# Optimization experiments

Measured on AMD Instinct MI355X. Metric: run time of the kernel, lower is better.

The kernel has to match this reference:

```python
import jax, jax.numpy as jnp
import numpy as np

B, S, DIM, NH, NKV, HD, HID, L, VOCAB = 1, 2048, 1024, 16, 8, 64, 2816, 2, 32000
EPS = 1e-5
SCALE = float(HD) ** 0.5
NEG = -255.0  # mask fill value used by executorch example inputs


def setup_inputs() -> dict:
    key = jax.random.key(0)
    ks = jax.random.split(key, 16)
    sd = 0.02
    def rnd(k, shape):
        return jax.random.normal(k, shape, dtype=jnp.float32) * sd
    # rope tables: precompute_freqs_cis(head_dim, max_seq_len)[: -1] -> [S, HD//2]
    inv = 1.0 / (10000.0 ** (np.arange(0, HD, 2, dtype=np.float32) / HD))
    ang = np.outer(np.arange(S, dtype=np.float32), inv)
    # causal mask [S, S]
    tril = np.tril(np.ones((S, S), dtype=bool))
    mask = np.where(tril, 0.0, NEG).astype(np.float32)
    return {
        "tokens": jax.random.randint(ks[0], (B, S), 0, VOCAB, dtype=jnp.int32),
        "atten_mask": jnp.asarray(mask),
        "freqs_cos": jnp.asarray(np.cos(ang)),
        "freqs_sin": jnp.asarray(np.sin(ang)),
        "tok_emb": rnd(ks[1], (VOCAB, DIM)),
        "wq": rnd(ks[2], (L, DIM, NH * HD)),
        "wk": rnd(ks[3], (L, DIM, NKV * HD)),
        "wv": rnd(ks[4], (L, DIM, NKV * HD)),
        "wo": rnd(ks[5], (L, NH * HD, DIM)),
        "attn_norm_w": jnp.ones((L, DIM), jnp.float32),
        "ffn_norm_w": jnp.ones((L, DIM), jnp.float32),
        "w1": rnd(ks[6], (L, DIM, HID)),
        "w2": rnd(ks[7], (L, HID, DIM)),
        "w3": rnd(ks[8], (L, DIM, HID)),
        "final_norm_w": jnp.ones((DIM,), jnp.float32),
        "out_w": rnd(ks[9], (DIM, VOCAB)),
    }


def _rmsnorm(x, w):
    return x * jax.lax.rsqrt(jnp.mean(x * x, axis=-1, keepdims=True) + EPS) * w


def _rope(x, c, s):
    # faithful to apply_rotary_emb_single: de-interleave, rotate, concat halves
    xr, xi = x[..., ::2], x[..., 1::2]          # [B,S,H,HD/2]
    c = c[None, :, None, :]
    s = s[None, :, None, :]
    return jnp.concatenate([xr * c - xi * s, xr * s + xi * c], axis=-1)


def reference(tokens, atten_mask, freqs_cos, freqs_sin, tok_emb, wq, wk, wv, wo,
              attn_norm_w, ffn_norm_w, w1, w2, w3, final_norm_w, out_w):
    rep = NH // NKV
    h = tok_emb[tokens]                           # [B,S,DIM]
    k_news, v_news = [], []
    for l in range(L):
        x = _rmsnorm(h, attn_norm_w[l])
        q = (x @ wq[l]).reshape(B, S, NH, HD)
        k = (x @ wk[l]).reshape(B, S, NKV, HD)
        v = (x @ wv[l]).reshape(B, S, NKV, HD)
        q = _rope(q, freqs_cos, freqs_sin)
        k = _rope(k, freqs_cos, freqs_sin)
        # GQA: each kv head serves NH//NKV query heads
        kr = jnp.repeat(k, rep, axis=2)           # [B,S,NH,HD]
        vr = jnp.repeat(v, rep, axis=2)
        attn = jnp.einsum('bshd,bthd->bhst', q, kr) / SCALE + atten_mask[None, None]
        p = jax.nn.softmax(attn, axis=-1)
        y = jnp.einsum('bhst,bthd->bshd', p, vr).reshape(B, S, NH * HD)
        h = h + y @ wo[l]
        x = _rmsnorm(h, ffn_norm_w[l])
        h = h + (jax.nn.silu(x @ w1[l]) * (x @ w3[l])) @ w2[l]
        # output_new_cache_only: last-position rotated K and raw V per kv head
        k_news.append(k[:, -1])                   # [B,NKV,HD]
        v_news.append(v[:, -1])
    logits = _rmsnorm(h, final_norm_w) @ out_w    # [B,S,VOCAB]
    return logits, jnp.stack(k_news), jnp.stack(v_news)
```

## Files before the change

kernel.cpp:

```cpp
#include <hip/hip_runtime.h>
#include <hip/hip_bf16.h>

typedef __bf16 bf16x8 __attribute__((ext_vector_type(8)));
typedef float f32x4 __attribute__((ext_vector_type(4)));
typedef unsigned short ushort4v __attribute__((ext_vector_type(4)));
typedef unsigned short ushort8v __attribute__((ext_vector_type(8)));

#define S_LEN 2048
#define DIM 1024
#define NH 16
#define NKV 8
#define HD 64
#define HID 2816
#define LOGITS ((size_t)S_LEN * 32000)

__device__ __forceinline__ unsigned short f2bf(float f) {
    union { float f; unsigned u; } v; v.f = f;
    unsigned r = v.u + 0x7fffu + ((v.u >> 16) & 1u);
    return (unsigned short)(r >> 16);
}
__device__ __forceinline__ float bf2f(unsigned short u) {
    union { unsigned u; float f; } v; v.u = (unsigned)u << 16; return v.f;
}

__device__ __forceinline__ void gload16(const unsigned short* g, unsigned short* l) {
    __builtin_amdgcn_global_load_lds(
        (const __attribute__((address_space(1))) unsigned int*)g,
        (__attribute__((address_space(3))) unsigned int*)l,
        16, 0, 0);
}

union Frag { f32x4 f; bf16x8 h; };

__device__ __forceinline__ f32x4 lds_read_b128(unsigned addr) {
    f32x4 d;
    asm volatile("ds_read_b128 %0, %1" : "=v"(d) : "v"(addr));
    return d;
}

#define BAR()  asm volatile("s_barrier" ::: "memory")
#define WAITV(n) asm volatile("s_waitcnt vmcnt(" #n ")" ::: "memory")
#define LGKM0() do { asm volatile("s_waitcnt lgkmcnt(0)" ::: "memory"); __builtin_amdgcn_sched_barrier(0); } while (0)

__global__ __launch_bounds__(256) void embed_kernel(const int* __restrict__ tokens,
                                                    const float* __restrict__ emb,
                                                    float* __restrict__ h) {
    int s = blockIdx.x;
    int t = tokens[s];
    float4 v = *(const float4*)&emb[(size_t)t * DIM + threadIdx.x * 4];
    *(float4*)&h[(size_t)s * DIM + threadIdx.x * 4] = v;
}

__global__ __launch_bounds__(256) void rmsnorm_kernel(const float* __restrict__ x,
                                                      const float* __restrict__ w,
                                                      unsigned short* __restrict__ out) {
    __shared__ float sred[4];
    int s = blockIdx.x;
    int tid = threadIdx.x;
    float4 v = *(const float4*)&x[(size_t)s * DIM + tid * 4];
    float ss = v.x * v.x + v.y * v.y + v.z * v.z + v.w * v.w;
#pragma unroll
    for (int off = 32; off; off >>= 1) ss += __shfl_down(ss, off);
    if ((tid & 63) == 0) sred[tid >> 6] = ss;
    __syncthreads();
    float tot = sred[0] + sred[1] + sred[2] + sred[3];
    float scale = rsqrtf(tot * (1.0f / DIM) + 1e-5f);
    float4 wv = *(const float4*)&w[tid * 4];
    ushort4v o;
    o[0] = f2bf(v.x * scale * wv.x); o[1] = f2bf(v.y * scale * wv.y);
    o[2] = f2bf(v.z * scale * wv.z); o[3] = f2bf(v.w * scale * wv.w);
    *(ushort4v*)&out[(size_t)s * DIM + tid * 4] = o;
}

__device__ __forceinline__ void tpose_body(const float* __restrict__ in,
                                           unsigned short* __restrict__ out,
                                           int K, int N, int n0, int k0,
                                           int rowMul, int rowOff) {
    __shared__ unsigned short t[64][68];
    int tid = threadIdx.x;
    int tn = tid & 15, tk = tid >> 4;
#pragma unroll
    for (int p = 0; p < 4; ++p) {
        int k = tk + p * 16;
        float4 v = *(const float4*)&in[(size_t)(k0 + k) * N + n0 + tn * 4];
        t[tn * 4 + 0][k] = f2bf(v.x);
        t[tn * 4 + 1][k] = f2bf(v.y);
        t[tn * 4 + 2][k] = f2bf(v.z);
        t[tn * 4 + 3][k] = f2bf(v.w);
    }
    __syncthreads();
    int wk = tid & 15, wn = tid >> 4;
#pragma unroll
    for (int p = 0; p < 4; ++p) {
        int n = wn + p * 16;
        ushort4v v;
        v[0] = t[n][wk * 4]; v[1] = t[n][wk * 4 + 1];
        v[2] = t[n][wk * 4 + 2]; v[3] = t[n][wk * 4 + 3];
        *(ushort4v*)&out[(size_t)(rowMul * (n0 + n) + rowOff) * K + k0 + wk * 4] = v;
    }
}

__global__ __launch_bounds__(256) void transpose_w(const float* __restrict__ in,
                                                   unsigned short* __restrict__ out,
                                                   int K, int N) {
    tpose_body(in, out, K, N, blockIdx.x * 64, blockIdx.y * 64, 1, 0);
}

__global__ __launch_bounds__(256) void transpose_qkv(const float* __restrict__ wq,
                                                     const float* __restrict__ wk,
                                                     const float* __restrict__ wv,
                                                     unsigned short* __restrict__ out) {
    int z = blockIdx.z;
    if (z > 0 && blockIdx.x >= 8) return;
    const float* in = z == 0 ? wq : (z == 1 ? wk : wv);
    int N = z == 0 ? 1024 : 512;
    int rowOff = z == 0 ? 0 : (z == 1 ? 1024 : 1536);
    tpose_body(in, out, DIM, N, blockIdx.x * 64, blockIdx.y * 64, 1, rowOff);
}

__global__ __launch_bounds__(256) void transpose_w13(const float* __restrict__ w1,
                                                     const float* __restrict__ w3,
                                                     unsigned short* __restrict__ out) {
    int z = blockIdx.z;
    tpose_body(z ? w3 : w1, out, DIM, HID, blockIdx.x * 64, blockIdx.y * 64, 2, z);
}

__global__ __launch_bounds__(256) void gemm_qkv(const unsigned short* __restrict__ A,
                                                const unsigned short* __restrict__ Bt,
                                                const float* __restrict__ fc,
                                                const float* __restrict__ fs,
                                                unsigned short* __restrict__ qb,
                                                unsigned short* __restrict__ kb,
                                                unsigned short* __restrict__ vT,
                                                float* __restrict__ out, int layer) {
    __shared__ unsigned short As[128 * 64];
    __shared__ unsigned short Bs[128 * 64];
    const int K = DIM, lda = DIM;
    int tid = threadIdx.x;
    int lane = tid & 63;
    int wid = tid >> 6;
    int wrow = wid >> 1, wcol = wid & 1;
    int lr = lane & 15, lg = lane >> 4;
    const int m0 = blockIdx.x * 128, n0 = blockIdx.y * 128;

    const int col8 = (((lane & 7) ^ ((lane >> 3) & 7)) * 8);
    const unsigned short* aG = A + (size_t)(m0 + wid * 32 + (lane >> 3)) * lda + col8;
    const unsigned short* bG = Bt + (size_t)(n0 + wid * 32 + (lane >> 3)) * K + col8;
    unsigned short* aL = As + wid * 2048;
    unsigned short* bL = Bs + wid * 2048;

    f32x4 acc[4][4] = {};

    for (int k0 = 0; k0 < K; k0 += 64) {
#pragma unroll
        for (int i = 0; i < 4; ++i)
            gload16(aG + (size_t)(i * 8) * lda + k0, aL + i * 512);
#pragma unroll
        for (int i = 0; i < 4; ++i)
            gload16(bG + (size_t)(i * 8) * K + k0, bL + i * 512);
        __syncthreads();
#pragma unroll
        for (int kk = 0; kk < 2; ++kk) {
            const int slot = ((kk * 4 + lg) ^ (lr & 7)) * 8;
            bf16x8 aF[4], bF[4];
#pragma unroll
            for (int mi = 0; mi < 4; ++mi)
                aF[mi] = *(const bf16x8*)&As[(wrow * 64 + mi * 16 + lr) * 64 + slot];
#pragma unroll
            for (int ni = 0; ni < 4; ++ni)
                bF[ni] = *(const bf16x8*)&Bs[(wcol * 64 + ni * 16 + lr) * 64 + slot];
#pragma unroll
            for (int mi = 0; mi < 4; ++mi)
#pragma unroll
                for (int ni = 0; ni < 4; ++ni)
                    acc[mi][ni] = __builtin_amdgcn_mfma_f32_16x16x32_bf16(aF[mi], bF[ni], acc[mi][ni], 0, 0, 0);
        }
        __syncthreads();
    }
#pragma unroll
    for (int mi = 0; mi < 4; ++mi)
#pragma unroll
        for (int ni = 0; ni < 4; ++ni) {
            int col = n0 + wcol * 64 + ni * 16 + lr;
            int s0r = m0 + wrow * 64 + mi * 16 + lg * 4;
            if (col < 1536) {
                int p = (col & 63) >> 1;
                int odd = col & 1;
#pragma unroll
                for (int r = 0; r < 4; ++r) {
                    float v = acc[mi][ni][r];
                    float o = __shfl_xor(v, 1);
                    int s = s0r + r;
                    float c = fc[s * 32 + p], sn = fs[s * 32 + p];
                    float res = odd ? (o * sn + v * c) : (v * c - o * sn);
                    int dpos = (odd ? 32 : 0) + p;
                    if (col < 1024) {
                        qb[(size_t)s * 1024 + (col >> 6) * 64 + dpos] = f2bf(res);
                    } else {
                        int kcol = ((col >> 6) - 16) * 64 + dpos;
                        kb[(size_t)s * 512 + kcol] = f2bf(res);
                        if (s == S_LEN - 1)
                            out[LOGITS + (size_t)layer * 512 + kcol] = res;
                    }
                }
            } else {
                int d = col - 1536;
                ushort4v vv;
#pragma unroll
                for (int r = 0; r < 4; ++r) vv[r] = f2bf(acc[mi][ni][r]);
                *(ushort4v*)&vT[(size_t)d * 2048 + s0r] = vv;
                if (s0r + 3 == S_LEN - 1)
                    out[LOGITS + 2 * 512 + (size_t)layer * 512 + d] = acc[mi][ni][3];
            }
        }
}

__global__ __launch_bounds__(256) void gemm_tn64(const unsigned short* __restrict__ A, int lda,
                                                 const unsigned short* __restrict__ Bt,
                                                 float* __restrict__ Cf,
                                                 const float* __restrict__ addsrc,
                                                 int N, int K) {
    __shared__ unsigned short As[64 * 64];
    __shared__ unsigned short Bs[128 * 64];
    int tid = threadIdx.x;
    int lane = tid & 63;
    int wid = tid >> 6;
    int lr = lane & 15, lg = lane >> 4;
    const int m0 = blockIdx.x * 64, n0 = blockIdx.y * 128;

    const int srow = tid >> 3;
    const int col8 = (((tid & 7) ^ ((tid >> 3) & 7)) * 8);
    const unsigned short* aG = A + (size_t)(m0 + srow) * lda + col8;
    const unsigned short* bG = Bt + (size_t)(n0 + srow) * K + col8;
    unsigned short* aL = As + wid * 512;
    unsigned short* bL = Bs + wid * 512;

    f32x4 acc[4][2] = {};

    for (int k0 = 0; k0 < K; k0 += 64) {
        gload16(aG + k0, aL);
        gload16(aG + (size_t)32 * lda + k0, aL + 2048);
#pragma unroll
        for (int i = 0; i < 4; ++i)
            gload16(bG + (size_t)(i * 32) * K + k0, bL + i * 2048);
        __syncthreads();
#pragma unroll
        for (int kk = 0; kk < 2; ++kk) {
            const int slot = ((kk * 4 + lg) ^ (lr & 7)) * 8;
            bf16x8 aF[4], bF[2];
#pragma unroll
            for (int mi = 0; mi < 4; ++mi)
                aF[mi] = *(const bf16x8*)&As[(mi * 16 + lr) * 64 + slot];
#pragma unroll
            for (int ni = 0; ni < 2; ++ni)
                bF[ni] = *(const bf16x8*)&Bs[(wid * 32 + ni * 16 + lr) * 64 + slot];
#pragma unroll
            for (int mi = 0; mi < 4; ++mi)
#pragma unroll
                for (int ni = 0; ni < 2; ++ni)
                    acc[mi][ni] = __builtin_amdgcn_mfma_f32_16x16x32_bf16(aF[mi], bF[ni], acc[mi][ni], 0, 0, 0);
        }
        __syncthreads();
    }
#pragma unroll
    for (int mi = 0; mi < 4; ++mi)
#pragma unroll
        for (int ni = 0; ni < 2; ++ni) {
            int row = m0 + mi * 16 + lg * 4;
            int col = n0 + wid * 32 + ni * 16 + lr;
#pragma unroll
            for (int r = 0; r < 4; ++r) {
                size_t idx = (size_t)(row + r) * N + col;
                float v = acc[mi][ni][r];
                if (addsrc) v += addsrc[idx];
                Cf[idx] = v;
            }
        }
}

template<int FUSE>
__global__ __launch_bounds__(512) void gemm8(const unsigned short* __restrict__ A,
                                             const unsigned short* __restrict__ Bt,
                                             float* __restrict__ Cf,
                                             unsigned short* __restrict__ Cb,
                                             int N, int K) {
    __shared__ unsigned short ldsbuf[65536];
    const int NT = K >> 6;
    int tid = threadIdx.x;
    int lane = tid & 63;
    int wid = tid >> 6;
    int wm = wid >> 2, wn = wid & 3;
    int lr = lane & 15, lg = lane >> 4;
    int wl = blockIdx.x * gridDim.y + blockIdx.y;
    const int m0 = (wl & 7) * 256, n0 = (wl >> 3) * 256;

    unsigned lds0 = (unsigned)(size_t)(__attribute__((address_space(3))) unsigned short*)ldsbuf;
    const unsigned xoff = (unsigned)((lg ^ ((lr >> 1) & 3)) * 16);
    const int gsw = (lane & 3) ^ ((lane >> 3) & 3);
    const int srow = wid * 16 + (lane >> 2);

#define STAGE(buf, ab, s, t) do {                                                   \
        const unsigned short* _src = (ab) ? Bt : A;                                 \
        int _r0 = (ab) ? n0 : m0;                                                   \
        unsigned short* _l = ldsbuf + (((buf) * 2 + (ab)) * 2 + (s)) * 8192 + wid * 512; \
        const unsigned short* _g = _src + (size_t)(_r0 + srow) * K + (size_t)(t) * 64 + (s) * 32 + gsw * 8; \
        gload16(_g, _l);                                                            \
        gload16(_g + (size_t)128 * K, _l + 4096);                                   \
    } while (0)

    f32x4 acc[8][4] = {};

    STAGE(0, 0, 0, 0); STAGE(0, 1, 0, 0);
    STAGE(0, 0, 1, 0); STAGE(0, 1, 1, 0);
    STAGE(1, 0, 0, 1); STAGE(1, 1, 0, 1);
    WAITV(8);
    BAR();

    for (int t = 0; t < NT; ++t) {
        int buf = t & 1;
        unsigned aBase = lds0 + (unsigned)(buf * 65536) + (unsigned)((wm * 128 + lr) * 64) + xoff;
        unsigned bBase = lds0 + (unsigned)(buf * 65536 + 32768) + (unsigned)((wn * 64 + lr) * 64) + xoff;
        Frag aF[4], bF[4];
#pragma unroll
        for (int s = 0; s < 2; ++s) {
#pragma unroll
            for (int ni = 0; ni < 4; ++ni)
                bF[ni].f = lds_read_b128(bBase + (unsigned)(s * 16384 + ni * 1024));
#pragma unroll
            for (int mi = 0; mi < 4; ++mi)
                aF[mi].f = lds_read_b128(aBase + (unsigned)(s * 16384 + mi * 1024));
            if (s == 0) { if (t + 1 < NT) STAGE(buf ^ 1, 0, 1, t + 1); }
            else        { if (t + 2 < NT) STAGE(buf,     0, 0, t + 2); }
            BAR();
            LGKM0();
            __builtin_amdgcn_s_setprio(1);
#pragma unroll
            for (int mi = 0; mi < 4; ++mi)
#pragma unroll
                for (int ni = 0; ni < 4; ++ni)
                    acc[mi][ni] = __builtin_amdgcn_mfma_f32_16x16x32_bf16(aF[mi].h, bF[ni].h, acc[mi][ni], 0, 0, 0);
            __builtin_amdgcn_s_setprio(0);
            BAR();
#pragma unroll
            for (int mi = 0; mi < 4; ++mi)
                aF[mi].f = lds_read_b128(aBase + (unsigned)(4096 + s * 16384 + mi * 1024));
            if (s == 0) { if (t + 1 < NT) STAGE(buf ^ 1, 1, 1, t + 1); }
            else        { if (t + 2 < NT) STAGE(buf,     1, 0, t + 2); }
            BAR();
            LGKM0();
            __builtin_amdgcn_s_setprio(1);
#pragma unroll
            for (int mi = 0; mi < 4; ++mi)
#pragma unroll
                for (int ni = 0; ni < 4; ++ni)
                    acc[4 + mi][ni] = __builtin_amdgcn_mfma_f32_16x16x32_bf16(aF[mi].h, bF[ni].h, acc[4 + mi][ni], 0, 0, 0);
            __builtin_amdgcn_s_setprio(0);
            if (s == 0) {
                if (t + 1 < NT) { WAITV(8); } else { WAITV(0); }
            } else {
                if (t + 2 < NT)      { WAITV(8); }
                else if (t + 1 < NT) { WAITV(4); }
            }
            BAR();
        }
    }
#undef STAGE

#pragma unroll
    for (int mi = 0; mi < 8; ++mi)
#pragma unroll
        for (int ni = 0; ni < 4; ++ni) {
            int row = m0 + wm * 128 + mi * 16 + lg * 4;
            int col = n0 + wn * 64 + ni * 16 + lr;
#pragma unroll
            for (int r = 0; r < 4; ++r) {
                float v = acc[mi][ni][r];
                if (FUSE) {
                    float o = __shfl_xor(v, 1);
                    if (!(lr & 1)) {
                        float res = v / (1.f + __expf(-v)) * o;
                        Cb[(size_t)(row + r) * (HID) + (col >> 1)] = f2bf(res);
                    }
                } else {
                    Cf[(size_t)(row + r) * N + col] = v;
                }
            }
        }
}

__global__ __launch_bounds__(512) void gemm8k32(const unsigned short* __restrict__ A,
                                                const unsigned short* __restrict__ Bt,
                                                float* __restrict__ Cf,
                                                int N, int K) {
    __shared__ unsigned short ldsbuf[32768];
    const int NT = K >> 5;
    int tid = threadIdx.x;
    int lane = tid & 63;
    int wid = tid >> 6;
    int wm = wid >> 2, wn = wid & 3;
    int lr = lane & 15, lg = lane >> 4;
    int wl = blockIdx.x * gridDim.y + blockIdx.y;
    const int m0 = (wl & 7) * 256, n0 = (wl >> 3) * 256;

    unsigned lds0 = (unsigned)(size_t)(__attribute__((address_space(3))) unsigned short*)ldsbuf;
    const unsigned xoff = (unsigned)((lg ^ ((lr >> 1) & 3)) * 16);
    const int gsw = (lane & 3) ^ ((lane >> 3) & 3);
    const int srow = wid * 16 + (lane >> 2);

#define STGA(t) do { \
        unsigned short* _l = ldsbuf + (((t) & 1) * 2 + 0) * 8192 + wid * 512; \
        const unsigned short* _g = A + (size_t)(m0 + srow) * K + (size_t)(t) * 32 + gsw * 8; \
        gload16(_g, _l); \
        gload16(_g + (size_t)128 * K, _l + 4096); \
    } while (0)
#define STGB(t) do { \
        unsigned short* _l = ldsbuf + (((t) & 1) * 2 + 1) * 8192 + wid * 512; \
        const unsigned short* _g = Bt + (size_t)(n0 + srow) * K + (size_t)(t) * 32 + gsw * 8; \
        gload16(_g, _l); \
        gload16(_g + (size_t)128 * K, _l + 4096); \
    } while (0)

    f32x4 acc[8][4] = {};

    STGA(0); STGB(0); STGB(1);
    WAITV(2);
    BAR();

    for (int t = 0; t < NT; ++t) {
        int buf = t & 1;
        unsigned aBase = lds0 + (unsigned)(buf * 32768) + (unsigned)((wm * 128 + lr) * 64) + xoff;
        unsigned bBase = lds0 + (unsigned)(buf * 32768 + 16384) + (unsigned)((wn * 64 + lr) * 64) + xoff;
        Frag aF[4], bF[4];
#pragma unroll
        for (int ni = 0; ni < 4; ++ni)
            bF[ni].f = lds_read_b128(bBase + (unsigned)(ni * 1024));
#pragma unroll
        for (int mi = 0; mi < 4; ++mi)
            aF[mi].f = lds_read_b128(aBase + (unsigned)(mi * 1024));
        if (t + 1 < NT) STGA(t + 1);
        BAR();
        LGKM0();
        __builtin_amdgcn_s_setprio(1);
#pragma unroll
        for (int mi = 0; mi < 4; ++mi)
#pragma unroll
            for (int ni = 0; ni < 4; ++ni)
                acc[mi][ni] = __builtin_amdgcn_mfma_f32_16x16x32_bf16(aF[mi].h, bF[ni].h, acc[mi][ni], 0, 0, 0);
        __builtin_amdgcn_s_setprio(0);
        BAR();
#pragma unroll
        for (int mi = 0; mi < 4; ++mi)
            aF[mi].f = lds_read_b128(aBase + (unsigned)(4096 + mi * 1024));
        if (t + 2 < NT) STGB(t + 2);
        BAR();
        LGKM0();
        __builtin_amdgcn_s_setprio(1);
#pragma unroll
        for (int mi = 0; mi < 4; ++mi)
#pragma unroll
            for (int ni = 0; ni < 4; ++ni)
                acc[4 + mi][ni] = __builtin_amdgcn_mfma_f32_16x16x32_bf16(aF[mi].h, bF[ni].h, acc[4 + mi][ni], 0, 0, 0);
        __builtin_amdgcn_s_setprio(0);
        if (t + 2 < NT)      { WAITV(2); }
        else if (t + 1 < NT) { WAITV(0); }
        BAR();
    }
#undef STGA
#undef STGB

#pragma unroll
    for (int mi = 0; mi < 8; ++mi)
#pragma unroll
        for (int ni = 0; ni < 4; ++ni) {
            int row = m0 + wm * 128 + mi * 16 + lg * 4;
            int col = n0 + wn * 64 + ni * 16 + lr;
#pragma unroll
            for (int r = 0; r < 4; ++r)
                Cf[(size_t)(row + r) * N + col] = acc[mi][ni][r];
        }
}

__global__ __launch_bounds__(256) void attn_kernel(const unsigned short* __restrict__ qb,
                                                   const unsigned short* __restrict__ kb,
                                                   const unsigned short* __restrict__ vT,
                                                   unsigned short* __restrict__ yb) {
    __shared__ unsigned short Klds[2][4096];
    __shared__ unsigned short Vlds[2][4096];
    __shared__ unsigned short P[4][16 * 72];
    int kvh = blockIdx.x;
    int strip = 63 - blockIdx.y;
    int tid = threadIdx.x;
    int lane = tid & 63;
    int w = tid >> 6;
    int hq = w & 1, qsub = w >> 1;
    int h = kvh * 2 + hq;
    int lr = lane & 15, lg = lane >> 4;
    int qbase = strip * 32 + qsub * 16;
    int qrow = qbase + lr;

    const int sr = tid >> 3;
    const int scol8 = (((tid & 7) ^ (sr & 7)) * 8);
    const int NT = (strip >> 1) + 1;

#define STAGEKV(buf, kt) do { \
        gload16(&kb[(size_t)((kt) * 64 + sr) * 512 + kvh * 64 + scol8], &Klds[buf][w * 512]); \
        gload16(&kb[(size_t)((kt) * 64 + sr + 32) * 512 + kvh * 64 + scol8], &Klds[buf][2048 + w * 512]); \
        gload16(&vT[(size_t)(kvh * 64 + sr) * 2048 + (kt) * 64 + scol8], &Vlds[buf][w * 512]); \
        gload16(&vT[(size_t)(kvh * 64 + sr + 32) * 2048 + (kt) * 64 + scol8], &Vlds[buf][2048 + w * 512]); \
    } while (0)

    bf16x8 bq[2];
#pragma unroll
    for (int c = 0; c < 2; ++c)
        bq[c] = *(const bf16x8*)&qb[(size_t)qrow * (NH * HD) + h * HD + c * 32 + lg * 8];

    f32x4 O[4] = {};
    float mstate = -1e30f, lstate = 0.f;

    STAGEKV(0, 0);
    WAITV(0);
    BAR();

    for (int kt = 0; kt < NT; ++kt) {
        int buf = kt & 1;
        if (kt + 1 < NT) STAGEKV(buf ^ 1, kt + 1);
        f32x4 s[4];
#pragma unroll
        for (int kc = 0; kc < 4; ++kc) {
            int krl = kc * 16 + lr;
            const unsigned short* kp = &Klds[buf][krl * 64];
            bf16x8 ak0 = *(const bf16x8*)&kp[((lg ^ (lr & 7)) * 8)];
            bf16x8 ak1 = *(const bf16x8*)&kp[(((4 + lg) ^ (lr & 7)) * 8)];
            f32x4 z = {};
            z = __builtin_amdgcn_mfma_f32_16x16x32_bf16(ak0, bq[0], z, 0, 0, 0);
            z = __builtin_amdgcn_mfma_f32_16x16x32_bf16(ak1, bq[1], z, 0, 0, 0);
            s[kc] = z;
        }
        float tm = -1e30f;
#pragma unroll
        for (int kc = 0; kc < 4; ++kc)
#pragma unroll
            for (int r = 0; r < 4; ++r) {
                int key = kt * 64 + kc * 16 + lg * 4 + r;
                float val = s[kc][r] * 0.125f;
                if (key > qrow) val = -1e30f;
                s[kc][r] = val;
                tm = fmaxf(tm, val);
            }
        tm = fmaxf(tm, __shfl_xor(tm, 16));
        tm = fmaxf(tm, __shfl_xor(tm, 32));
        float mn = fmaxf(mstate, tm);
        float sc = __expf(mstate - mn);
        float rs = 0.f;
        ushort4v pk[4];
#pragma unroll
        for (int kc = 0; kc < 4; ++kc)
#pragma unroll
            for (int r = 0; r < 4; ++r) {
                float pf = __expf(s[kc][r] - mn);
                rs += pf;
                pk[kc][r] = f2bf(pf);
            }
        rs += __shfl_xor(rs, 16);
        rs += __shfl_xor(rs, 32);
        lstate = lstate * sc + rs;
        mstate = mn;
        float osc[4];
#pragma unroll
        for (int r = 0; r < 4; ++r)
            osc[r] = __shfl(sc, lg * 4 + r);
#pragma unroll
        for (int n = 0; n < 4; ++n)
#pragma unroll
            for (int r = 0; r < 4; ++r)
                O[n][r] *= osc[r];
#pragma unroll
        for (int kc = 0; kc < 4; ++kc)
            *(ushort4v*)&P[w][lr * 72 + kc * 16 + lg * 4] = pk[kc];
        bf16x8 pa[2];
#pragma unroll
        for (int g = 0; g < 2; ++g)
            pa[g] = *(const bf16x8*)&P[w][lr * 72 + g * 32 + lg * 8];
#pragma unroll
        for (int n = 0; n < 4; ++n) {
            const unsigned short* vp = &Vlds[buf][(n * 16 + lr) * 64];
#pragma unroll
            for (int g = 0; g < 2; ++g) {
                bf16x8 bv = *(const bf16x8*)&vp[(((g * 4 + lg) ^ (lr & 7)) * 8)];
                O[n] = __builtin_amdgcn_mfma_f32_16x16x32_bf16(pa[g], bv, O[n], 0, 0, 0);
            }
        }
        if (kt + 1 < NT) WAITV(0);
        LGKM0();
        BAR();
    }
#undef STAGEKV

    float linv[4];
#pragma unroll
    for (int r = 0; r < 4; ++r)
        linv[r] = 1.f / __shfl(lstate, lg * 4 + r);
#pragma unroll
    for (int n = 0; n < 4; ++n)
#pragma unroll
        for (int r = 0; r < 4; ++r) {
            int row = qbase + lg * 4 + r;
            yb[(size_t)row * (NH * HD) + h * HD + n * 16 + lr] = f2bf(O[n][r] * linv[r]);
        }
}

extern "C" void kernel_launch(void* const* d_in, const int* in_sizes, int n_in,
                              void* d_out, int out_size, void* d_ws, size_t ws_size,
                              hipStream_t stream) {
    const int* tokens = (const int*)d_in[0];
    const float* freqs_cos = (const float*)d_in[2];
    const float* freqs_sin = (const float*)d_in[3];
    const float* tok_emb = (const float*)d_in[4];
    const float* wq = (const float*)d_in[5];
    const float* wk = (const float*)d_in[6];
    const float* wv = (const float*)d_in[7];
    const float* wo = (const float*)d_in[8];
    const float* attn_norm_w = (const float*)d_in[9];
    const float* ffn_norm_w = (const float*)d_in[10];
    const float* w1 = (const float*)d_in[11];
    const float* w2 = (const float*)d_in[12];
    const float* w3 = (const float*)d_in[13];
    const float* final_norm_w = (const float*)d_in[14];
    const float* out_w = (const float*)d_in[15];
    float* out = (float*)d_out;

    const size_t SD = (size_t)S_LEN * DIM;
    const size_t SKV = (size_t)S_LEN * NKV * HD;

    char* p = (char*)d_ws;
    auto take = [&](size_t bytes) { char* r = p; p += (bytes + 255) & ~(size_t)255; return r; };
    float* h            = (float*)take(SD * 4);
    unsigned short* xnb = (unsigned short*)take(SD * 2);
    char* uni = p;
    unsigned short* qb  = (unsigned short*)uni;
    unsigned short* kb  = qb + SD;
    unsigned short* vT  = kb + SKV;
    unsigned short* ybv = vT + SKV;
    unsigned short* gu  = ybv + SD;
    unsigned short* wT  = gu + (size_t)S_LEN * HID;
    unsigned short* owT = (unsigned short*)uni;

    embed_kernel<<<S_LEN, 256, 0, stream>>>(tokens, tok_emb, h);
    for (int l = 0; l < 2; ++l) {
        rmsnorm_kernel<<<S_LEN, 256, 0, stream>>>(h, attn_norm_w + l * DIM, xnb);
        transpose_qkv<<<dim3(16, 16, 3), 256, 0, stream>>>(
            wq + (size_t)l * DIM * 1024, wk + (size_t)l * DIM * 512, wv + (size_t)l * DIM * 512, wT);
        gemm_qkv<<<dim3(16, 16), 256, 0, stream>>>(xnb, wT, freqs_cos, freqs_sin,
                                                   qb, kb, vT, out, l);
        attn_kernel<<<dim3(NKV, 64), 256, 0, stream>>>(qb, kb, vT, ybv);
        transpose_w<<<dim3(16, 16), 256, 0, stream>>>(wo + (size_t)l * 1024 * DIM, wT, 1024, DIM);
        gemm_tn64<<<dim3(32, 8), 256, 0, stream>>>(ybv, 1024, wT, h, h, DIM, 1024);
        rmsnorm_kernel<<<S_LEN, 256, 0, stream>>>(h, ffn_norm_w + l * DIM, xnb);
        transpose_w13<<<dim3(44, 16, 2), 256, 0, stream>>>(
            w1 + (size_t)l * DIM * HID, w3 + (size_t)l * DIM * HID, wT);
        gemm8<1><<<dim3(8, 22), 512, 0, stream>>>(xnb, wT, nullptr, gu, 5632, DIM);
        transpose_w<<<dim3(16, 44), 256, 0, stream>>>(w2 + (size_t)l * HID * 1024, wT, HID, 1024);
        gemm_tn64<<<dim3(32, 8), 256, 0, stream>>>(gu, HID, wT, h, h, DIM, HID);
    }
    rmsnorm_kernel<<<S_LEN, 256, 0, stream>>>(h, final_norm_w, xnb);
    transpose_w<<<dim3(500, 16), 256, 0, stream>>>(out_w, owT, DIM, 32000);
    gemm8k32<<<dim3(8, 125), 512, 0, stream>>>(xnb, owT, out, 32000, DIM);
}
```

Before: 648.2 us.

## Merge per-layer weight transposes, double-buffer GEMMs, replace gemm8 with 128-tile kernel

All seven per-layer weight transposes now run in one launch that writes into separate buffers, which removes several kernel launches and the serialization between them. The qkv and tn64 GEMMs gain double-buffered LDS staging, so the next k-tile's global loads overlap the current tile's MFMAs with one barrier per step. The hand-scheduled 256x256 gemm8 kernel for the fused w1/w3 SiLU GEMM is replaced by a simpler double-buffered 128x128 gemm_tn128. That kernel may have less data reuse and lose gemm8's fine-grained interleaving, and the larger LDS footprint can lower occupancy.

Measured after the change: 631.5 us, median of 2. 2.6% less time.

```diff
diff --git a/kernel.cpp b/kernel.cpp
--- a/kernel.cpp
+++ b/kernel.cpp
@@ -106,23 +106,39 @@
     tpose_body(in, out, K, N, blockIdx.x * 64, blockIdx.y * 64, 1, 0);
 }
 
-__global__ __launch_bounds__(256) void transpose_qkv(const float* __restrict__ wq,
-                                                     const float* __restrict__ wk,
-                                                     const float* __restrict__ wv,
-                                                     unsigned short* __restrict__ out) {
-    int z = blockIdx.z;
-    if (z > 0 && blockIdx.x >= 8) return;
-    const float* in = z == 0 ? wq : (z == 1 ? wk : wv);
-    int N = z == 0 ? 1024 : 512;
-    int rowOff = z == 0 ? 0 : (z == 1 ? 1024 : 1536);
-    tpose_body(in, out, DIM, N, blockIdx.x * 64, blockIdx.y * 64, 1, rowOff);
-}
-
-__global__ __launch_bounds__(256) void transpose_w13(const float* __restrict__ w1,
-                                                     const float* __restrict__ w3,
-                                                     unsigned short* __restrict__ out) {
-    int z = blockIdx.z;
-    tpose_body(z ? w3 : w1, out, DIM, HID, blockIdx.x * 64, blockIdx.y * 64, 2, z);
+__global__ __launch_bounds__(256) void transpose_layer(const float* __restrict__ wq,
+                                                       const float* __restrict__ wk,
+                                                       const float* __restrict__ wv,
+                                                       const float* __restrict__ wo,
+                                                       const float* __restrict__ w1,
+                                                       const float* __restrict__ w3,
+                                                       const float* __restrict__ w2,
+                                                       unsigned short* __restrict__ wTqkv,
+                                                       unsigned short* __restrict__ wTo,
+                                                       unsigned short* __restrict__ wT13,
+                                                       unsigned short* __restrict__ wT2) {
+    int id = blockIdx.x;
+    if (id < 256) {
+        tpose_body(wq, wTqkv, 1024, 1024, (id & 15) * 64, (id >> 4) * 64, 1, 0);
+    } else if (id < 384) {
+        int i = id - 256;
+        tpose_body(wk, wTqkv, 1024, 512, (i & 7) * 64, (i >> 3) * 64, 1, 1024);
+    } else if (id < 512) {
+        int i = id - 384;
+        tpose_body(wv, wTqkv, 1024, 512, (i & 7) * 64, (i >> 3) * 64, 1, 1536);
+    } else if (id < 768) {
+        int i = id - 512;
+        tpose_body(wo, wTo, 1024, 1024, (i & 15) * 64, (i >> 4) * 64, 1, 0);
+    } else if (id < 1472) {
+        int i = id - 768;
+        tpose_body(w1, wT13, 1024, HID, (i % 44) * 64, (i / 44) * 64, 2, 0);
+    } else if (id < 2176) {
+        int i = id - 1472;
+        tpose_body(w3, wT13, 1024, HID, (i % 44) * 64, (i / 44) * 64, 2, 1);
+    } else {
+        int i = id - 2176;
+        tpose_body(w2, wT2, 2816, 1024, (i & 15) * 64, (i >> 4) * 64, 1, 0);
+    }
 }
 
 __global__ __launch_bounds__(256) void gemm_qkv(const unsigned short* __restrict__ A,
@@ -133,8 +149,8 @@
                                                 unsigned short* __restrict__ kb,
                                                 unsigned short* __restrict__ vT,
                                                 float* __restrict__ out, int layer) {
-    __shared__ unsigned short As[128 * 64];
-    __shared__ unsigned short Bs[128 * 64];
+    __shared__ unsigned short As[2][128 * 64];
+    __shared__ unsigned short Bs[2][128 * 64];
     const int K = DIM, lda = DIM;
     int tid = threadIdx.x;
     int lane = tid & 63;
@@ -146,37 +162,47 @@
     const int col8 = (((lane & 7) ^ ((lane >> 3) & 7)) * 8);
     const unsigned short* aG = A + (size_t)(m0 + wid * 32 + (lane >> 3)) * lda + col8;
     const unsigned short* bG = Bt + (size_t)(n0 + wid * 32 + (lane >> 3)) * K + col8;
-    unsigned short* aL = As + wid * 2048;
-    unsigned short* bL = Bs + wid * 2048;
+    const int NT = K >> 6;
+
+#define STG128(buf, k0) do {                                                  \
+        unsigned short* _aL = &As[buf][wid * 2048];                           \
+        unsigned short* _bL = &Bs[buf][wid * 2048];                           \
+        _Pragma("unroll")                                                     \
+        for (int _i = 0; _i < 4; ++_i) {                                      \
+            gload16(aG + (size_t)(_i * 8) * lda + (k0), _aL + _i * 512);      \
+            gload16(bG + (size_t)(_i * 8) * K + (k0), _bL + _i * 512);        \
+        }                                                                     \
+    } while (0)
 
     f32x4 acc[4][4] = {};
-
-    for (int k0 = 0; k0 < K; k0 += 64) {
-#pragma unroll
-        for (int i = 0; i < 4; ++i)
-            gload16(aG + (size_t)(i * 8) * lda + k0, aL + i * 512);
-#pragma unroll
-        for (int i = 0; i < 4; ++i)
-            gload16(bG + (size_t)(i * 8) * K + k0, bL + i * 512);
-        __syncthreads();
+    STG128(0, 0);
+    WAITV(0);
+    BAR();
+
+    for (int t = 0; t < NT; ++t) {
+        int buf = t & 1;
+        if (t + 1 < NT) STG128(buf ^ 1, (t + 1) * 64);
 #pragma unroll
         for (int kk = 0; kk < 2; ++kk) {
             const int slot = ((kk * 4 + lg) ^ (lr & 7)) * 8;
             bf16x8 aF[4], bF[4];
 #pragma unroll
             for (int mi = 0; mi < 4; ++mi)
-                aF[mi] = *(const bf16x8*)&As[(wrow * 64 + mi * 16 + lr) * 64 + slot];
+                aF[mi] = *(const bf16x8*)&As[buf][(wrow * 64 + mi * 16 + lr) * 64 + slot];
 #pragma unroll
             for (int ni = 0; ni < 4; ++ni)
-                bF[ni] = *(const bf16x8*)&Bs[(wcol * 64 + ni * 16 + lr) * 64 + slot];
+                bF[ni] = *(const bf16x8*)&Bs[buf][(wcol * 64 + ni * 16 + lr) * 64 + slot];
 #pragma unroll
             for (int mi = 0; mi < 4; ++mi)
 #pragma unroll
                 for (int ni = 0; ni < 4; ++ni)
                     acc[mi][ni] = __builtin_amdgcn_mfma_f32_16x16x32_bf16(aF[mi], bF[ni], acc[mi][ni], 0, 0, 0);
         }
-        __syncthreads();
-    }
+        if (t + 1 < NT) WAITV(0);
+        BAR();
+    }
+#undef STG128
+
 #pragma unroll
     for (int mi = 0; mi < 4; ++mi)
 #pragma unroll
@@ -215,13 +241,96 @@
         }
 }
 
+template<int FUSE>
+__global__ __launch_bounds__(256) void gemm_tn128(const unsigned short* __restrict__ A, int lda,
+                                                  const unsigned short* __restrict__ Bt,
+                                                  float* __restrict__ Cf,
+                                                  unsigned short* __restrict__ Cb,
+                                                  const float* __restrict__ addsrc,
+                                                  int N, int K) {
+    __shared__ unsigned short As[2][128 * 64];
+    __shared__ unsigned short Bs[2][128 * 64];
+    int tid = threadIdx.x;
+    int lane = tid & 63;
+    int wid = tid >> 6;
+    int wrow = wid >> 1, wcol = wid & 1;
+    int lr = lane & 15, lg = lane >> 4;
+    const int m0 = blockIdx.x * 128, n0 = blockIdx.y * 128;
+
+    const int col8 = (((lane & 7) ^ ((lane >> 3) & 7)) * 8);
+    const unsigned short* aG = A + (size_t)(m0 + wid * 32 + (lane >> 3)) * lda + col8;
+    const unsigned short* bG = Bt + (size_t)(n0 + wid * 32 + (lane >> 3)) * K + col8;
+    const int NT = K >> 6;
+
+#define STG128(buf, k0) do {                                                  \
+        unsigned short* _aL = &As[buf][wid * 2048];                           \
+        unsigned short* _bL = &Bs[buf][wid * 2048];                           \
+        _Pragma("unroll")                                                     \
+        for (int _i = 0; _i < 4; ++_i) {                                      \
+            gload16(aG + (size_t)(_i * 8) * lda + (k0), _aL + _i * 512);      \
+            gload16(bG + (size_t)(_i * 8) * K + (k0), _bL + _i * 512);        \
+        }                                                                     \
+    } while (0)
+
+    f32x4 acc[4][4] = {};
+    STG128(0, 0);
+    WAITV(0);
+    BAR();
+
+    for (int t = 0; t < NT; ++t) {
+        int buf = t & 1;
+        if (t + 1 < NT) STG128(buf ^ 1, (t + 1) * 64);
+#pragma unroll
+        for (int kk = 0; kk < 2; ++kk) {
+            const int slot = ((kk * 4 + lg) ^ (lr & 7)) * 8;
+            bf16x8 aF[4], bF[4];
+#pragma unroll
+            for (int mi = 0; mi < 4; ++mi)
+                aF[mi] = *(const bf16x8*)&As[buf][(wrow * 64 + mi * 16 + lr) * 64 + slot];
+#pragma unroll
+            for (int ni = 0; ni < 4; ++ni)
+                bF[ni] = *(const bf16x8*)&Bs[buf][(wcol * 64 + ni * 16 + lr) * 64 + slot];
+#pragma unroll
+            for (int mi = 0; mi < 4; ++mi)
+#pragma unroll
+                for (int ni = 0; ni < 4; ++ni)
+                    acc[mi][ni] = __builtin_amdgcn_mfma_f32_16x16x32_bf16(aF[mi], bF[ni], acc[mi][ni], 0, 0, 0);
+        }
+        if (t + 1 < NT) WAITV(0);
+        BAR();
+    }
+#undef STG128
+
+#pragma unroll
+    for (int mi = 0; mi < 4; ++mi)
+#pragma unroll
+        for (int ni = 0; ni < 4; ++ni) {
+            int row = m0 + wrow * 64 + mi * 16 + lg * 4;
+            int col = n0 + wcol * 64 + ni * 16 + lr;
+#pragma unroll
+            for (int r = 0; r < 4; ++r) {
+                float v = acc[mi][ni][r];
+                if (FUSE) {
+                    float o = __shfl_xor(v, 1);
+                    if (!(lr & 1))
+                        Cb[(size_t)(row + r) * HID + (col >> 1)] = f2bf(v / (1.f + __expf(-v)) * o);
+                } else {
+                    size_t idx = (size_t)(row + r) * N + col;
+                    if (addsrc) v += addsrc[idx];
+                    if (Cb) Cb[idx] = f2bf(v);
+                    else    Cf[idx] = v;
+                }
+            }
+        }
+}
+
 __global__ __launch_bounds__(256) void gemm_tn64(const unsigned short* __restrict__ A, int lda,
                                                  const unsigned short* __restrict__ Bt,
                                                  float* __restrict__ Cf,
                                                  const float* __restrict__ addsrc,
                                                  int N, int K) {
-    __shared__ unsigned short As[64 * 64];
-    __shared__ unsigned short Bs[128 * 64];
+    __shared__ unsigned short As[2][64 * 64];
+    __shared__ unsigned short Bs[2][128 * 64];
     int tid = threadIdx.x;
     int lane = tid & 63;
     int wid = tid >> 6;
@@ -232,36 +341,45 @@
     const int col8 = (((tid & 7) ^ ((tid >> 3) & 7)) * 8);
     const unsigned short* aG = A + (size_t)(m0 + srow) * lda + col8;
     const unsigned short* bG = Bt + (size_t)(n0 + srow) * K + col8;
-    unsigned short* aL = As + wid * 512;
-    unsigned short* bL = Bs + wid * 512;
+    const int NT = K >> 6;
+
+#define STG64(buf, k0) do {                                                   \
+        gload16(aG + (k0), &As[buf][wid * 512]);                              \
+        gload16(aG + (size_t)32 * lda + (k0), &As[buf][wid * 512 + 2048]);    \
+        _Pragma("unroll")                                                     \
+        for (int _i = 0; _i < 4; ++_i)                                        \
+            gload16(bG + (size_t)(_i * 32) * K + (k0), &Bs[buf][wid * 512 + _i * 2048]); \
+    } while (0)
 
     f32x4 acc[4][2] = {};
-
-    for (int k0 = 0; k0 < K; k0 += 64) {
-        gload16(aG + k0, aL);
-        gload16(aG + (size_t)32 * lda + k0, aL + 2048);
-#pragma unroll
-        for (int i = 0; i < 4; ++i)
-            gload16(bG + (size_t)(i * 32) * K + k0, bL + i * 2048);
-        __syncthreads();
+    STG64(0, 0);
+    WAITV(0);
+    BAR();
+
+    for (int t = 0; t < NT; ++t) {
+        int buf = t & 1;
+        if (t + 1 < NT) STG64(buf ^ 1, (t + 1) * 64);
 #pragma unroll
         for (int kk = 0; kk < 2; ++kk) {
             const int slot = ((kk * 4 + lg) ^ (lr & 7)) * 8;
             bf16x8 aF[4], bF[2];
 #pragma unroll
             for (int mi = 0; mi < 4; ++mi)
-                aF[mi] = *(const bf16x8*)&As[(mi * 16 + lr) * 64 + slot];
+                aF[mi] = *(const bf16x8*)&As[buf][(mi * 16 + lr) * 64 + slot];
 #pragma unroll
             for (int ni = 0; ni < 2; ++ni)
-                bF[ni] = *(const bf16x8*)&Bs[(wid * 32 + ni * 16 + lr) * 64 + slot];
+                bF[ni] = *(const bf16x8*)&Bs[buf][(wid * 32 + ni * 16 + lr) * 64 + slot];
 #pragma unroll
             for (int mi = 0; mi < 4; ++mi)
 #pragma unroll
                 for (int ni = 0; ni < 2; ++ni)
                     acc[mi][ni] = __builtin_amdgcn_mfma_f32_16x16x32_bf16(aF[mi], bF[ni], acc[mi][ni], 0, 0, 0);
         }
-        __syncthreads();
-    }
+        if (t + 1 < NT) WAITV(0);
+        BAR();
+    }
+#undef STG64
+
 #pragma unroll
     for (int mi = 0; mi < 4; ++mi)
 #pragma unroll
@@ -274,116 +392,6 @@
                 float v = acc[mi][ni][r];
                 if (addsrc) v += addsrc[idx];
                 Cf[idx] = v;
-            }
-        }
-}
-
-template<int FUSE>
-__global__ __launch_bounds__(512) void gemm8(const unsigned short* __restrict__ A,
-                                             const unsigned short* __restrict__ Bt,
-                                             float* __restrict__ Cf,
-                                             unsigned short* __restrict__ Cb,
-                                             int N, int K) {
-    __shared__ unsigned short ldsbuf[65536];
-    const int NT = K >> 6;
-    int tid = threadIdx.x;
-    int lane = tid & 63;
-    int wid = tid >> 6;
-    int wm = wid >> 2, wn = wid & 3;
-    int lr = lane & 15, lg = lane >> 4;
-    int wl = blockIdx.x * gridDim.y + blockIdx.y;
-    const int m0 = (wl & 7) * 256, n0 = (wl >> 3) * 256;
-
-    unsigned lds0 = (unsigned)(size_t)(__attribute__((address_space(3))) unsigned short*)ldsbuf;
-    const unsigned xoff = (unsigned)((lg ^ ((lr >> 1) & 3)) * 16);
-    const int gsw = (lane & 3) ^ ((lane >> 3) & 3);
-    const int srow = wid * 16 + (lane >> 2);
-
-#define STAGE(buf, ab, s, t) do {                                                   \
-        const unsigned short* _src = (ab) ? Bt : A;                                 \
-        int _r0 = (ab) ? n0 : m0;                                                   \
-        unsigned short* _l = ldsbuf + (((buf) * 2 + (ab)) * 2 + (s)) * 8192 + wid * 512; \
-        const unsigned short* _g = _src + (size_t)(_r0 + srow) * K + (size_t)(t) * 64 + (s) * 32 + gsw * 8; \
-        gload16(_g, _l);                                                            \
-        gload16(_g + (size_t)128 * K, _l + 4096);                                   \
-    } while (0)
-
-    f32x4 acc[8][4] = {};
-
-    STAGE(0, 0, 0, 0); STAGE(0, 1, 0, 0);
-    STAGE(0, 0, 1, 0); STAGE(0, 1, 1, 0);
-    STAGE(1, 0, 0, 1); STAGE(1, 1, 0, 1);
-    WAITV(8);
-    BAR();
-
-    for (int t = 0; t < NT; ++t) {
-        int buf = t & 1;
-        unsigned aBase = lds0 + (unsigned)(buf * 65536) + (unsigned)((wm * 128 + lr) * 64) + xoff;
-        unsigned bBase = lds0 + (unsigned)(buf * 65536 + 32768) + (unsigned)((wn * 64 + lr) * 64) + xoff;
-        Frag aF[4], bF[4];
-#pragma unroll
-        for (int s = 0; s < 2; ++s) {
-#pragma unroll
-            for (int ni = 0; ni < 4; ++ni)
-                bF[ni].f = lds_read_b128(bBase + (unsigned)(s * 16384 + ni * 1024));
-#pragma unroll
-            for (int mi = 0; mi < 4; ++mi)
-                aF[mi].f = lds_read_b128(aBase + (unsigned)(s * 16384 + mi * 1024));
-            if (s == 0) { if (t + 1 < NT) STAGE(buf ^ 1, 0, 1, t + 1); }
-            else        { if (t + 2 < NT) STAGE(buf,     0, 0, t + 2); }
-            BAR();
-            LGKM0();
-            __builtin_amdgcn_s_setprio(1);
-#pragma unroll
-            for (int mi = 0; mi < 4; ++mi)
-#pragma unroll
-                for (int ni = 0; ni < 4; ++ni)
-                    acc[mi][ni] = __builtin_amdgcn_mfma_f32_16x16x32_bf16(aF[mi].h, bF[ni].h, acc[mi][ni], 0, 0, 0);
-            __builtin_amdgcn_s_setprio(0);
-            BAR();
-#pragma unroll
-            for (int mi = 0; mi < 4; ++mi)
-                aF[mi].f = lds_read_b128(aBase + (unsigned)(4096 + s * 16384 + mi * 1024));
-            if (s == 0) { if (t + 1 < NT) STAGE(buf ^ 1, 1, 1, t + 1); }
-            else        { if (t + 2 < NT) STAGE(buf,     1, 0, t + 2); }
-            BAR();
-            LGKM0();
-            __builtin_amdgcn_s_setprio(1);
-#pragma unroll
-            for (int mi = 0; mi < 4; ++mi)
-#pragma unroll
-                for (int ni = 0; ni < 4; ++ni)
-                    acc[4 + mi][ni] = __builtin_amdgcn_mfma_f32_16x16x32_bf16(aF[mi].h, bF[ni].h, acc[4 + mi][ni], 0, 0, 0);
-            __builtin_amdgcn_s_setprio(0);
-            if (s == 0) {
-                if (t + 1 < NT) { WAITV(8); } else { WAITV(0); }
-            } else {
-                if (t + 2 < NT)      { WAITV(8); }
-                else if (t + 1 < NT) { WAITV(4); }
-            }
-            BAR();
-        }
-    }
-#undef STAGE
-
-#pragma unroll
-    for (int mi = 0; mi < 8; ++mi)
-#pragma unroll
-        for (int ni = 0; ni < 4; ++ni) {
-            int row = m0 + wm * 128 + mi * 16 + lg * 4;
-            int col = n0 + wn * 64 + ni * 16 + lr;
-#pragma unroll
-            for (int r = 0; r < 4; ++r) {
-                float v = acc[mi][ni][r];
-                if (FUSE) {
-                    float o = __shfl_xor(v, 1);
-                    if (!(lr & 1)) {
-                        float res = v / (1.f + __expf(-v)) * o;
-                        Cb[(size_t)(row + r) * (HID) + (col >> 1)] = f2bf(res);
-                    }
-                } else {
-                    Cf[(size_t)(row + r) * N + col] = v;
-                }
             }
         }
 }
@@ -637,30 +645,32 @@
     float* h            = (float*)take(SD * 4);
     unsigned short* xnb = (unsigned short*)take(SD * 2);
     char* uni = p;
-    unsigned short* qb  = (unsigned short*)uni;
-    unsigned short* kb  = qb + SD;
-    unsigned short* vT  = kb + SKV;
-    unsigned short* ybv = vT + SKV;
-    unsigned short* gu  = ybv + SD;
-    unsigned short* wT  = gu + (size_t)S_LEN * HID;
-    unsigned short* owT = (unsigned short*)uni;
+    unsigned short* qb    = (unsigned short*)uni;
+    unsigned short* kb    = qb + SD;
+    unsigned short* vT    = kb + SKV;
+    unsigned short* ybv   = vT + SKV;
+    unsigned short* gu    = ybv + SD;
+    unsigned short* wTqkv = gu + (size_t)S_LEN * HID;
+    unsigned short* wTo   = wTqkv + (size_t)2048 * DIM;
+    unsigned short* wT13  = wTo + (size_t)DIM * DIM;
+    unsigned short* wT2   = wT13 + (size_t)2 * HID * DIM;
+    unsigned short* owT   = (unsigned short*)uni;
 
     embed_kernel<<<S_LEN, 256, 0, stream>>>(tokens, tok_emb, h);
     for (int l = 0; l < 2; ++l) {
         rmsnorm_kernel<<<S_LEN, 256, 0, stream>>>(h, attn_norm_w + l * DIM, xnb);
-        transpose_qkv<<<dim3(16, 16, 3), 256, 0, stream>>>(
-            wq + (size_t)l * DIM * 1024, wk + (size_t)l * DIM * 512, wv + (size_t)l * DIM * 512, wT);
-        gemm_qkv<<<dim3(16, 16), 256, 0, stream>>>(xnb, wT, freqs_cos, freqs_sin,
+        transpose_layer<<<2880, 256, 0, stream>>>(
+            wq + (size_t)l * DIM * 1024, wk + (size_t)l * DIM * 512, wv + (size_t)l * DIM * 512,
+            wo + (size_t)l * 1024 * DIM,
+            w1 + (size_t)l * DIM * HID, w3 + (size_t)l * DIM * HID, w2 + (size_t)l * HID * 1024,
+            wTqkv, wTo, wT13, wT2);
+        gemm_qkv<<<dim3(16, 16), 256, 0, stream>>>(xnb, wTqkv, freqs_cos, freqs_sin,
                                                    qb, kb, vT, out, l);
         attn_kernel<<<dim3(NKV, 64), 256, 0, stream>>>(qb, kb, vT, ybv);
-        transpose_w<<<dim3(16, 16), 256, 0, stream>>>(wo + (size_t)l * 1024 * DIM, wT, 1024, DIM);
-        gemm_tn64<<<dim3(32, 8), 256, 0, stream>>>(ybv, 1024, wT, h, h, DIM, 1024);
+        gemm_tn64<<<dim3(32, 8), 256, 0, stream>>>(ybv, 1024, wTo, h, h, DIM, 1024);
         rmsnorm_kernel<<<S_LEN, 256, 0, stream>>>(h, ffn_norm_w + l * DIM, xnb);
-        transpose_w13<<<dim3(44, 16, 2), 256, 0, stream>>>(
-            w1 + (size_t)l * DIM * HID, w3 + (size_t)l * DIM * HID, wT);
-        gemm8<1><<<dim3(8, 22), 512, 0, stream>>>(xnb, wT, nullptr, gu, 5632, DIM);
-        transpose_w<<<dim3(16, 44), 256, 0, stream>>>(w2 + (size_t)l * HID * 1024, wT, HID, 1024);
-        gemm_tn64<<<dim3(32, 8), 256, 0, stream>>>(gu, HID, wT, h, h, DIM, HID);
+        gemm_tn128<1><<<dim3(16, 44), 256, 0, stream>>>(xnb, DIM, wT13, nullptr, gu, nullptr, 5632, DIM);
+        gemm_tn64<<<dim3(32, 8), 256, 0, stream>>>(gu, HID, wT2, h, h, DIM, HID);
     }
     rmsnorm_kernel<<<S_LEN, 256, 0, stream>>>(h, final_norm_w, xnb);
     transpose_w<<<dim3(500, 16), 256, 0, stream>>>(out_w, owT, DIM, 32000);
```
